# Performance work log

Hardware: AMD Instinct MI355X
Metric: run time of the kernel (lower is better)

## Reference

```python
import jax, jax.numpy as jnp
import numpy as np

SH_C0 = 0.28209479177387814
SH_C1 = 0.4886025119029199
SH_C2 = (1.0925484305920792, -1.0925484305920792, 0.31539156525252005, -1.0925484305920792, 0.5462742152960396)
SH_C3 = (-0.5900435899266435, 2.890611442640554, -0.4570457994644658, 0.3731763325901154, -0.4570457994644658, 1.445305721320277, -0.5900435899266435)

BG = 128  # gaussians per compositing block


def quat_to_rot(q):
    # q: [N,4] normalized quaternion (w,x,y,z) -> [N,3,3]
    w, x, y, z = q[:, 0], q[:, 1], q[:, 2], q[:, 3]
    R = jnp.stack([
        1 - 2 * (y * y + z * z), 2 * (x * y - w * z), 2 * (x * z + w * y),
        2 * (x * y + w * z), 1 - 2 * (x * x + z * z), 2 * (y * z - w * x),
        2 * (x * z - w * y), 2 * (y * z + w * x), 1 - 2 * (x * x + y * y)],
        axis=-1)
    return R.reshape(-1, 3, 3)


def eval_sh(sh, d):
    # sh: [N,16,3] degree-3 SH coeffs; d: [N,3] unit view dirs -> [N,3] rgb
    x, y, z = d[:, 0:1], d[:, 1:2], d[:, 2:3]
    xx, yy, zz = x * x, y * y, z * z
    xy, yz, xz = x * y, y * z, x * z
    res = SH_C0 * sh[:, 0]
    res = res - SH_C1 * y * sh[:, 1] + SH_C1 * z * sh[:, 2] - SH_C1 * x * sh[:, 3]
    res = (res + SH_C2[0] * xy * sh[:, 4] + SH_C2[1] * yz * sh[:, 5]
           + SH_C2[2] * (2 * zz - xx - yy) * sh[:, 6]
           + SH_C2[3] * xz * sh[:, 7] + SH_C2[4] * (xx - yy) * sh[:, 8])
    res = (res + SH_C3[0] * y * (3 * xx - yy) * sh[:, 9] + SH_C3[1] * xy * z * sh[:, 10]
           + SH_C3[2] * y * (4 * zz - xx - yy) * sh[:, 11]
           + SH_C3[3] * z * (2 * zz - 3 * xx - 3 * yy) * sh[:, 12]
           + SH_C3[4] * x * (4 * zz - xx - yy) * sh[:, 13]
           + SH_C3[5] * z * (xx - yy) * sh[:, 14] + SH_C3[6] * x * (xx - 3 * yy) * sh[:, 15])
    return res


def gs_forward(pws, shs, alphas_raw, scales_raw, rots_raw, us, Rcw, tcw, intr, height, width):
    fx, fy, cx, cy = intr[0], intr[1], intr[2], intr[3]
    N = pws.shape[0]
    HW = height * width

    # activations (GSModel.forward)
    alphas = jax.nn.sigmoid(alphas_raw[:, 0])          # [N]
    scales = jnp.exp(scales_raw)                       # [N,3]
    rots = rots_raw / jnp.linalg.norm(rots_raw, axis=1, keepdims=True)

    # gsc.project
    pcs = pws @ Rcw.T + tcw                            # [N,3] camera frame
    depth = pcs[:, 2]
    zs = jnp.where(depth > 0.2, depth, 1.0)            # safe divide for culled pts
    u = jnp.stack([fx * pcs[:, 0] / zs + cx, fy * pcs[:, 1] / zs + cy], axis=-1)
    # the `us` input is a grad-capture dummy; forward value comes from projection
    u = u + us - jax.lax.stop_gradient(us)

    # gsc.computeCov3D: Cov3d = (R S)(R S)^T
    R = quat_to_rot(rots)
    M = R * scales[:, None, :]
    cov3d = M @ jnp.swapaxes(M, 1, 2)                  # [N,3,3]

    # gsc.computeCov2D: cov2d = J W Cov3d W^T J^T + 0.3 I
    tanfx = width / (2.0 * fx)
    tanfy = height / (2.0 * fy)
    tx = jnp.clip(pcs[:, 0] / zs, -1.3 * tanfx, 1.3 * tanfx) * zs
    ty = jnp.clip(pcs[:, 1] / zs, -1.3 * tanfy, 1.3 * tanfy) * zs
    zero = jnp.zeros_like(zs)
    J = jnp.stack([
        fx / zs, zero, -fx * tx / (zs * zs),
        zero, fy / zs, -fy * ty / (zs * zs)], axis=-1).reshape(N, 2, 3)
    T = jnp.einsum('nij,jk->nik', J, Rcw)              # [N,2,3]
    cov2d = jnp.einsum('nij,njk,nlk->nil', T, cov3d, T)
    cov2d = cov2d + 0.3 * jnp.eye(2, dtype=cov2d.dtype)
    a, b, c = cov2d[:, 0, 0], cov2d[:, 0, 1], cov2d[:, 1, 1]
    det = a * c - b * b
    valid = (depth > 0.2) & (det > 0)
    det_s = jnp.where(valid, det, 1.0)

    # gsc.inverseCov2D: conic + screen-space radius (areas)
    cinv = jnp.stack([c / det_s, -b / det_s, a / det_s], axis=-1)  # [N,3]
    mid = 0.5 * (a + c)
    lam = mid + jnp.sqrt(jnp.maximum(mid * mid - det, 0.1))
    radius = jnp.where(valid, jnp.ceil(3.0 * jnp.sqrt(lam)), 0.0)
    areas = jnp.stack([radius, radius], axis=-1)       # [N,2]

    # gsc.sh2Color
    twc = -Rcw.T @ tcw
    dirs = pws - twc
    dirs = dirs / jnp.linalg.norm(dirs, axis=1, keepdims=True)
    colors = jnp.maximum(eval_sh(shs.reshape(N, 16, 3), dirs) + 0.5, 0.0)  # [N,3]

    # gsc.splat: depth-sorted front-to-back alpha compositing over all pixels
    order = jnp.argsort(depth)
    nb = N // BG
    u_s = u[order].reshape(nb, BG, 2)
    cinv_s = cinv[order].reshape(nb, BG, 3)
    al_s = alphas[order].reshape(nb, BG)
    col_s = colors[order].reshape(nb, BG, 3)
    val_s = valid[order].reshape(nb, BG)

    ys, xs = jnp.meshgrid(jnp.arange(height, dtype=jnp.float32),
                          jnp.arange(width, dtype=jnp.float32), indexing='ij')
    px = xs.ravel()
    py = ys.ravel()

    @jax.checkpoint
    def body(carry, blk):
        logT, acc = carry                              # [HW], [3,HW]
        ub, cb, ab, colb, vb = blk
        dx = px[None, :] - ub[:, 0:1]                  # [BG,HW]
        dy = py[None, :] - ub[:, 1:2]
        power = -0.5 * (cb[:, 0:1] * dx * dx + cb[:, 2:3] * dy * dy) - cb[:, 1:2] * dx * dy
        alp = jnp.minimum(0.99, ab[:, None] * jnp.exp(power))
        alp = jnp.where((power <= 0) & (alp >= 1.0 / 255.0) & vb[:, None], alp, 0.0)
        l1m = jnp.log1p(-alp)
        cs = jnp.cumsum(l1m, axis=0)
        logT_i = logT[None, :] + jnp.concatenate(
            [jnp.zeros((1, HW), l1m.dtype), cs[:-1]], axis=0)  # exclusive transmittance
        Ti = jnp.exp(logT_i)
        w = jnp.where(Ti > 1e-4, alp * Ti, 0.0)        # early-termination at tau<1e-4
        acc = acc + jnp.einsum('gp,gc->cp', w, colb)
        return (logT + cs[-1], acc), None

    init = (jnp.zeros(HW, dtype=jnp.float32), jnp.zeros((3, HW), dtype=jnp.float32))
    (_, acc), _ = jax.lax.scan(body, init, (u_s, cinv_s, al_s, col_s, val_s))
    image = acc.reshape(3, height, width)
    return image, areas


def setup_inputs() -> dict:
    key = jax.random.key(0)
    ks = jax.random.split(key, 6)
    N, H, W = 8192, 256, 256
    pws = jax.random.normal(ks[0], (N, 3), jnp.float32) * 2.0 + jnp.array([0.0, 0.0, 6.0])
    shs = jax.random.normal(ks[1], (N, 48), jnp.float32) * 0.3
    alphas_raw = jax.random.normal(ks[2], (N, 1), jnp.float32)
    scales_raw = jax.random.normal(ks[3], (N, 3), jnp.float32) * 0.3 - 3.0
    rots_raw = jax.random.normal(ks[4], (N, 4), jnp.float32)
    us = jnp.zeros((N, 2), jnp.float32)
    Rcw = jnp.eye(3, dtype=jnp.float32)
    tcw = jnp.zeros((3,), jnp.float32)
    intr = jnp.array([400.0, 400.0, 128.0, 128.0], jnp.float32)  # fx, fy, cx, cy
    return {"pws": pws, "shs": shs, "alphas_raw": alphas_raw, "scales_raw": scales_raw,
            "rots_raw": rots_raw, "us": us, "Rcw": Rcw, "tcw": tcw, "intr": intr,
            "height": H, "width": W}


def reference(pws, shs, alphas_raw, scales_raw, rots_raw, us, Rcw, tcw, intr, height, width):
    return gs_forward(pws, shs, alphas_raw, scales_raw, rots_raw, us, Rcw, tcw, intr, height, width)
```

## Files before the change

kernel.cpp:

```cpp
#include <hip/hip_runtime.h>

__global__ __launch_bounds__(64) void k_pre(
    const float* __restrict__ pws, const float* __restrict__ shs,
    const float* __restrict__ alphas_raw, const float* __restrict__ scales_raw,
    const float* __restrict__ rots_raw, const float* __restrict__ Rcw,
    const float* __restrict__ tcw, const float* __restrict__ intr,
    int N, int W, int H, float* __restrict__ areas,
    unsigned long long* __restrict__ keys, unsigned* __restrict__ rank,
    float* __restrict__ P)
{
    int i = blockIdx.x * 64 + threadIdx.x;
    if (i >= N) return;
    rank[i] = 0u;

    float R00=Rcw[0],R01=Rcw[1],R02=Rcw[2];
    float R10=Rcw[3],R11=Rcw[4],R12=Rcw[5];
    float R20=Rcw[6],R21=Rcw[7],R22=Rcw[8];
    float t0=tcw[0],t1=tcw[1],t2=tcw[2];
    float fx=intr[0],fy=intr[1],cx=intr[2],cy=intr[3];

    float pwx=pws[i*3+0], pwy=pws[i*3+1], pwz=pws[i*3+2];
    float pcx = R00*pwx + R01*pwy + R02*pwz + t0;
    float pcy = R10*pwx + R11*pwy + R12*pwz + t1;
    float pcz = R20*pwx + R21*pwy + R22*pwz + t2;
    float depth = pcz;
    float zs = (depth > 0.2f) ? depth : 1.0f;
    float u0 = fx * pcx / zs + cx;
    float u1 = fy * pcy / zs + cy;

    float4 q4 = *reinterpret_cast<const float4*>(rots_raw + i*4);
    float qw=q4.x, qx=q4.y, qy=q4.z, qz=q4.w;
    float qn = sqrtf(qw*qw + qx*qx + qy*qy + qz*qz);
    qw/=qn; qx/=qn; qy/=qn; qz/=qn;
    float s0 = expf(scales_raw[i*3+0]);
    float s1 = expf(scales_raw[i*3+1]);
    float s2 = expf(scales_raw[i*3+2]);

    float xx=qx*qx, yy=qy*qy, zq=qz*qz;
    float xy=qx*qy, xz=qx*qz, yz=qy*qz;
    float wx=qw*qx, wy=qw*qy, wz=qw*qz;
    float r00=1.f-2.f*(yy+zq), r01=2.f*(xy-wz),     r02=2.f*(xz+wy);
    float r10=2.f*(xy+wz),     r11=1.f-2.f*(xx+zq), r12=2.f*(yz-wx);
    float r20=2.f*(xz-wy),     r21=2.f*(yz+wx),     r22=1.f-2.f*(xx+yy);

    float m00=r00*s0, m01=r01*s1, m02=r02*s2;
    float m10=r10*s0, m11=r11*s1, m12=r12*s2;
    float m20=r20*s0, m21=r21*s1, m22=r22*s2;
    float V00=m00*m00+m01*m01+m02*m02;
    float V01=m00*m10+m01*m11+m02*m12;
    float V02=m00*m20+m01*m21+m02*m22;
    float V11=m10*m10+m11*m11+m12*m12;
    float V12=m10*m20+m11*m21+m12*m22;
    float V22=m20*m20+m21*m21+m22*m22;

    float tanfx = (float)W / (2.f*fx), tanfy = (float)H / (2.f*fy);
    float limx = 1.3f*tanfx, limy = 1.3f*tanfy;
    float txl = fminf(fmaxf(pcx/zs, -limx), limx) * zs;
    float tyl = fminf(fmaxf(pcy/zs, -limy), limy) * zs;
    float iz = 1.f/zs, iz2 = iz*iz;
    float J00 = fx*iz, J02 = -fx*txl*iz2;
    float J11 = fy*iz, J12 = -fy*tyl*iz2;

    float T00=J00*R00+J02*R20, T01=J00*R01+J02*R21, T02=J00*R02+J02*R22;
    float T10=J11*R10+J12*R20, T11=J11*R11+J12*R21, T12=J11*R12+J12*R22;
    float A0=T00*V00+T01*V01+T02*V02;
    float A1=T00*V01+T01*V11+T02*V12;
    float A2=T00*V02+T01*V12+T02*V22;
    float B0=T10*V00+T11*V01+T12*V02;
    float B1=T10*V01+T11*V11+T12*V12;
    float B2=T10*V02+T11*V12+T12*V22;
    float ca = A0*T00+A1*T01+A2*T02 + 0.3f;
    float cb = A0*T10+A1*T11+A2*T12;
    float cc = B0*T10+B1*T11+B2*T12 + 0.3f;

    float det = ca*cc - cb*cb;
    bool valid = (depth > 0.2f) && (det > 0.f);
    float det_s = valid ? det : 1.f;
    float dinv = 1.f/det_s;
    float ci0 =  cc*dinv, ci1 = -cb*dinv, ci2 = ca*dinv;
    float mid = 0.5f*(ca+cc);
    float lam = mid + sqrtf(fmaxf(mid*mid - det, 0.1f));
    float radius = valid ? ceilf(3.f*sqrtf(lam)) : 0.f;
    areas[2*i+0] = radius;
    areas[2*i+1] = radius;

    float alpha = 1.f/(1.f + expf(-alphas_raw[i]));

    float tw0 = -(R00*t0 + R10*t1 + R20*t2);
    float tw1 = -(R01*t0 + R11*t1 + R21*t2);
    float tw2 = -(R02*t0 + R12*t1 + R22*t2);
    float dx_=pwx-tw0, dy_=pwy-tw1, dz_=pwz-tw2;
    float dn = sqrtf(dx_*dx_+dy_*dy_+dz_*dz_);
    float x=dx_/dn, y=dy_/dn, z=dz_/dn;
    float sxx=x*x, syy=y*y, szz=z*z;
    float sxy=x*y, syz=y*z, sxz=x*z;

    float shl[48];
    const float4* sh4 = reinterpret_cast<const float4*>(shs + i*48);
    #pragma unroll
    for (int k = 0; k < 12; ++k) {
        float4 v = sh4[k];
        shl[4*k+0]=v.x; shl[4*k+1]=v.y; shl[4*k+2]=v.z; shl[4*k+3]=v.w;
    }
    float col[3];
    #pragma unroll
    for (int c = 0; c < 3; ++c) {
        float res = 0.28209479177387814f*shl[0*3+c];
        res += -0.4886025119029199f*y*shl[1*3+c]
             +  0.4886025119029199f*z*shl[2*3+c]
             + -0.4886025119029199f*x*shl[3*3+c];
        res +=  1.0925484305920792f*sxy*shl[4*3+c]
             + -1.0925484305920792f*syz*shl[5*3+c]
             +  0.31539156525252005f*(2.f*szz-sxx-syy)*shl[6*3+c]
             + -1.0925484305920792f*sxz*shl[7*3+c]
             +  0.5462742152960396f*(sxx-syy)*shl[8*3+c];
        res += -0.5900435899266435f*y*(3.f*sxx-syy)*shl[9*3+c]
             +  2.890611442640554f*sxy*z*shl[10*3+c]
             + -0.4570457994644658f*y*(4.f*szz-sxx-syy)*shl[11*3+c]
             +  0.3731763325901154f*z*(2.f*szz-3.f*sxx-3.f*syy)*shl[12*3+c]
             + -0.4570457994644658f*x*(4.f*szz-sxx-syy)*shl[13*3+c]
             +  1.445305721320277f*z*(sxx-syy)*shl[14*3+c]
             + -0.5900435899266435f*x*(sxx-3.f*syy)*shl[15*3+c];
        col[c] = fmaxf(res + 0.5f, 0.f);
    }

    float rc2;
    if (!valid || 255.f*alpha < 0.999f) {
        rc2 = -1.f;
    } else {
        float r2 = 2.f*lam*logf(255.f*alpha);
        float r  = sqrtf(fmaxf(r2, 0.f)) + 1.f;
        rc2 = r*r;
    }

    P[0*N+i]=u0;  P[1*N+i]=u1;  P[2*N+i]=ci0; P[3*N+i]=ci1; P[4*N+i]=ci2;
    P[5*N+i]=alpha; P[6*N+i]=col[0]; P[7*N+i]=col[1]; P[8*N+i]=col[2];
    P[9*N+i]=rc2;

    unsigned ud = __float_as_uint(depth);
    ud = (ud & 0x80000000u) ? ~ud : (ud | 0x80000000u);
    keys[i] = ((unsigned long long)ud << 32) | (unsigned)i;
}

#define JC 512
__global__ __launch_bounds__(256) void k_rank_scatter(
    const unsigned long long* __restrict__ keys, int N,
    unsigned* __restrict__ rank, const float* __restrict__ Pun,
    float4* __restrict__ gA, float4* __restrict__ gB,
    float4* __restrict__ cull)
{
    __shared__ unsigned long long sk[JC];
    const int j0 = blockIdx.y * JC;
    const int nJ = gridDim.y;
    for (int t = threadIdx.x; t < JC; t += 256) {
        int j = j0 + t;
        sk[t] = (j < N) ? keys[j] : ~0ull;
    }
    __syncthreads();

    const int i = blockIdx.x * 256 + threadIdx.x;
    unsigned long long my = (i < N) ? keys[i] : 0ull;

    int c = 0;
    const ulonglong2* sk2 = (const ulonglong2*)sk;
    #pragma unroll 4
    for (int t = 0; t < JC/2; ++t) {
        ulonglong2 kk = sk2[t];
        c += (kk.x < my) ? 1 : 0;
        c += (kk.y < my) ? 1 : 0;
    }
    if (i < N) {
        unsigned old = atomicAdd(&rank[i], (unsigned)c + (1u << 20));
        if ((int)(old >> 20) == nJ - 1) {
            int s = (int)(old & 0xFFFFFu) + c;
            cull[s] = make_float4(Pun[0*N+i], Pun[1*N+i], Pun[9*N+i], 0.f);
            gA[s]   = make_float4(Pun[2*N+i], Pun[3*N+i], Pun[4*N+i], Pun[5*N+i]);
            gB[s]   = make_float4(Pun[6*N+i], Pun[7*N+i], Pun[8*N+i], 0.f);
        }
    }
}

__global__ __launch_bounds__(256, 8) void k_render(
    const float4* __restrict__ gA, const float4* __restrict__ gB,
    const float4* __restrict__ cull, int N, int W, int H,
    int nSuper, int superX, int tilesX, int tilesY, int nseg,
    float4* __restrict__ segbuf)
{
    const int tid  = threadIdx.x;
    const int wv   = tid >> 6, lane = tid & 63;
    const int sup  = blockIdx.x % nSuper, seg = blockIdx.x / nSuper;
    const int sX   = sup % superX, sY = sup / superX;
    const int tX   = (sX << 1) + (wv & 1);
    const int tY   = (sY << 1) + (wv >> 1);
    const bool tOK = (tX < tilesX) && (tY < tilesY);
    const int ix = (tX << 3) + (lane & 7);
    const int iy = (tY << 3) + (lane >> 3);
    const bool inb = tOK && (ix < W) && (iy < H);
    const float pxf = (float)ix, pyf = (float)iy;
    const float tx0 = (float)(tX << 3), ty0 = (float)(tY << 3);
    int tx1i = (tX << 3) + 7; if (tx1i > W-1) tx1i = W-1;
    int ty1i = (tY << 3) + 7; if (ty1i > H-1) ty1i = H-1;
    const float tx1 = (float)tx1i, ty1 = (float)ty1i;

    const int per = (N + nseg - 1) / nseg;
    const int g0 = seg * per;
    const int g1 = min(N, g0 + per);

    float T = inb ? 1.f : 0.f;
    float aR = 0.f, aG = 0.f, aB = 0.f;

    __shared__ float4 sG0[4][64];
    __shared__ float4 sG1[4][64];
    __shared__ float  sB2[4][64];

    if (tOK) {
        for (int base = g0; base < g1; base += 64) {
            int g = base + lane;
            bool ov = false;
            float u0 = 0.f, u1 = 0.f;
            if (g < g1) {
                float4 cu = cull[g];
                u0 = cu.x; u1 = cu.y;
                float cxp = fminf(fmaxf(u0, tx0), tx1);
                float cyp = fminf(fmaxf(u1, ty0), ty1);
                float ddx = u0 - cxp, ddy = u1 - cyp;
                ov = (ddx*ddx + ddy*ddy) <= cu.z;
            }
            unsigned long long m = __ballot(ov);
            int cnt = __popcll(m);
            if (ov) {
                int pos = __popcll(m & ((1ull << lane) - 1ull));
                float4 a4 = gA[g];
                float4 b4 = gB[g];
                sG0[wv][pos] = make_float4(u0, u1, a4.x, a4.y);
                sG1[wv][pos] = make_float4(a4.z, a4.w, b4.x, b4.y);
                sB2[wv][pos] = b4.z;
            }
            for (int e = 0; e < cnt; ++e) {
                float4 e0 = sG0[wv][e];
                float4 e1 = sG1[wv][e];
                float  gb = sB2[wv][e];
                float ddx = pxf - e0.x, ddy = pyf - e0.y;
                float power = -0.5f*(e0.z*ddx*ddx + e1.x*ddy*ddy) - e0.w*ddx*ddy;
                float alp = fminf(0.99f, e1.y * __expf(power));
                alp = (power <= 0.f && alp >= (1.0f/255.0f)) ? alp : 0.f;
                float w = (T > 0.0001f) ? alp * T : 0.f;
                aR = fmaf(w, e1.z, aR);
                aG = fmaf(w, e1.w, aG);
                aB = fmaf(w, gb, aB);
                T = T - T * alp;
            }
            if (__all(T <= 0.0001f)) break;
        }
    }

    if (inb) {
        int pix = iy * W + ix;
        segbuf[(size_t)seg * (size_t)(W*H) + pix] = make_float4(T, aR, aG, aB);
    }
}

__global__ __launch_bounds__(256) void k_combine(
    const float4* __restrict__ segbuf, int HW, int nseg,
    float* __restrict__ out)
{
    int p = blockIdx.x * 256 + threadIdx.x;
    if (p >= HW) return;
    float T = 1.f, r = 0.f, g = 0.f, b = 0.f;
    for (int s = 0; s < nseg; ++s) {
        float4 v = segbuf[(size_t)s * HW + p];
        r = fmaf(T, v.y, r);
        g = fmaf(T, v.z, g);
        b = fmaf(T, v.w, b);
        T *= v.x;
    }
    out[p] = r; out[HW + p] = g; out[2*HW + p] = b;
}

extern "C" void kernel_launch(void* const* d_in, const int* in_sizes, int n_in,
                              void* d_out, int out_size, void* d_ws, size_t ws_size,
                              hipStream_t stream) {
    const float* pws        = (const float*)d_in[0];
    const float* shs        = (const float*)d_in[1];
    const float* alphas_raw = (const float*)d_in[2];
    const float* scales_raw = (const float*)d_in[3];
    const float* rots_raw   = (const float*)d_in[4];
    const float* Rcw        = (const float*)d_in[6];
    const float* tcw        = (const float*)d_in[7];
    const float* intr       = (const float*)d_in[8];

    const int N  = in_sizes[0] / 3;
    const int HW = (out_size - 2 * N) / 3;
    int W = 1; while ((long long)W * W < (long long)HW) ++W;
    const int H = HW / W;

    float* out   = (float*)d_out;
    float* areas = out + 3 * HW;

    char* ws = (char*)d_ws;
    size_t off = 0;
    unsigned long long* keys = (unsigned long long*)(ws + off); off += (size_t)N * 8;
    unsigned* rank = (unsigned*)(ws + off);                     off += (size_t)N * 4;
    off = (off + 15) & ~(size_t)15;
    float* Pun = (float*)(ws + off);                            off += (size_t)10 * N * 4;
    off = (off + 15) & ~(size_t)15;
    float4* cullv = (float4*)(ws + off);                        off += (size_t)N * 16;
    float4* gA = (float4*)(ws + off);                           off += (size_t)N * 16;
    float4* gB = (float4*)(ws + off);                           off += (size_t)N * 16;
    float4* segbuf = (float4*)(ws + off);
    size_t remain = (ws_size > off) ? (ws_size - off) : 0;
    int nseg = 8;
    while (nseg > 1 && (size_t)nseg * (size_t)HW * 16 > remain) nseg >>= 1;

    k_pre<<<(N + 63) / 64, 64, 0, stream>>>(pws, shs, alphas_raw, scales_raw,
                                            rots_raw, Rcw, tcw, intr, N, W, H,
                                            areas, keys, rank, Pun);
    dim3 rgrid((N + 255) / 256, (N + JC - 1) / JC);
    k_rank_scatter<<<rgrid, 256, 0, stream>>>(keys, N, rank, Pun, gA, gB, cullv);
    int tilesX = (W + 7) / 8, tilesY = (H + 7) / 8;
    int superX = (tilesX + 1) / 2, superY = (tilesY + 1) / 2;
    int nSuper = superX * superY;
    k_render<<<nSuper * nseg, 256, 0, stream>>>(gA, gB, cullv, N, W, H,
                                                nSuper, superX, tilesX, tilesY,
                                                nseg, segbuf);
    k_combine<<<(HW + 255) / 256, 256, 0, stream>>>(segbuf, HW, nseg, out);
}
```

Before: 108.4 us.

## Prefetch next gaussian chunk into registers and broadcast via wave shuffles

The compositing loop now loads the next 64-gaussian chunk's cull, gA and gB data into registers one iteration ahead, so global load latency overlaps the current chunk's blending. It also drops the shared-memory compaction staging and broadcasts each overlapping gaussian's parameters from its owning lane with __shfl, walking the ballot mask with ffs. The aim is to remove LDS writes and reads and expose memory-level parallelism. The cost is more register pressure, nine cross-lane shuffles per composited gaussian, and loading gA/gB for every gaussian rather than only the overlapping ones.

```diff
diff --git a/kernel.cpp b/kernel.cpp
--- a/kernel.cpp
+++ b/kernel.cpp
@@ -209,48 +209,53 @@
     float T = inb ? 1.f : 0.f;
     float aR = 0.f, aG = 0.f, aB = 0.f;
 
-    __shared__ float4 sG0[4][64];
-    __shared__ float4 sG1[4][64];
-    __shared__ float  sB2[4][64];
-
     if (tOK) {
+        int gl0 = min(g0 + lane, N - 1);
+        float4 cu = cull[gl0];
+        float4 a4 = gA[gl0];
+        float4 b4 = gB[gl0];
+
         for (int base = g0; base < g1; base += 64) {
+            float4 cu_n = make_float4(0.f, 0.f, -1.f, 0.f);
+            float4 a4_n = make_float4(0.f, 0.f, 0.f, 0.f);
+            float4 b4_n = make_float4(0.f, 0.f, 0.f, 0.f);
+            if (base + 64 < g1) {
+                int gln = min(base + 64 + lane, N - 1);
+                cu_n = cull[gln];
+                a4_n = gA[gln];
+                b4_n = gB[gln];
+            }
+
             int g = base + lane;
             bool ov = false;
-            float u0 = 0.f, u1 = 0.f;
             if (g < g1) {
-                float4 cu = cull[g];
-                u0 = cu.x; u1 = cu.y;
-                float cxp = fminf(fmaxf(u0, tx0), tx1);
-                float cyp = fminf(fmaxf(u1, ty0), ty1);
-                float ddx = u0 - cxp, ddy = u1 - cyp;
+                float cxp = fminf(fmaxf(cu.x, tx0), tx1);
+                float cyp = fminf(fmaxf(cu.y, ty0), ty1);
+                float ddx = cu.x - cxp, ddy = cu.y - cyp;
                 ov = (ddx*ddx + ddy*ddy) <= cu.z;
             }
-            unsigned long long m = __ballot(ov);
-            int cnt = __popcll(m);
-            if (ov) {
-                int pos = __popcll(m & ((1ull << lane) - 1ull));
-                float4 a4 = gA[g];
-                float4 b4 = gB[g];
-                sG0[wv][pos] = make_float4(u0, u1, a4.x, a4.y);
-                sG1[wv][pos] = make_float4(a4.z, a4.w, b4.x, b4.y);
-                sB2[wv][pos] = b4.z;
-            }
-            for (int e = 0; e < cnt; ++e) {
-                float4 e0 = sG0[wv][e];
-                float4 e1 = sG1[wv][e];
-                float  gb = sB2[wv][e];
-                float ddx = pxf - e0.x, ddy = pyf - e0.y;
-                float power = -0.5f*(e0.z*ddx*ddx + e1.x*ddy*ddy) - e0.w*ddx*ddy;
-                float alp = fminf(0.99f, e1.y * __expf(power));
+
+            unsigned long long mm = __ballot(ov);
+            while (mm) {
+                int l = __ffsll(mm) - 1;
+                mm &= mm - 1ull;
+                float su0 = __shfl(cu.x, l), su1 = __shfl(cu.y, l);
+                float ci0 = __shfl(a4.x, l), ci1 = __shfl(a4.y, l);
+                float ci2 = __shfl(a4.z, l), sal = __shfl(a4.w, l);
+                float cr  = __shfl(b4.x, l), cg  = __shfl(b4.y, l);
+                float cbv = __shfl(b4.z, l);
+                float ddx = pxf - su0, ddy = pyf - su1;
+                float power = -0.5f*(ci0*ddx*ddx + ci2*ddy*ddy) - ci1*ddx*ddy;
+                float alp = fminf(0.99f, sal * __expf(power));
                 alp = (power <= 0.f && alp >= (1.0f/255.0f)) ? alp : 0.f;
                 float w = (T > 0.0001f) ? alp * T : 0.f;
-                aR = fmaf(w, e1.z, aR);
-                aG = fmaf(w, e1.w, aG);
-                aB = fmaf(w, gb, aB);
+                aR = fmaf(w, cr, aR);
+                aG = fmaf(w, cg, aG);
+                aB = fmaf(w, cbv, aB);
                 T = T - T * alp;
             }
             if (__all(T <= 0.0001f)) break;
+            cu = cu_n; a4 = a4_n; b4 = b4_n;
         }
     }
 
```

Result: no change. 108.1 us (-0.3%).
